# Optimization experiments

Hardware: AMD Instinct MI355X
Metric: run time of the kernel (lower is better)

The kernel has to match this reference:

```python
import jax, jax.numpy as jnp
import numpy as np

B, T, W = 64, 64, 20
VIDEO_DIM = 1024
JOINT_DIM = 1024
K, STRIDE = 4, 4
MARGIN = 0.2
EPS = 1e-8


def _l2norm(x, axis=-1):
    n = jnp.sqrt(jnp.sum(x * x, axis=axis, keepdims=True))
    return x / jnp.maximum(n, EPS)


def _conv1d(x, w, b, stride):
    # x: (B, C, L), w: (O, I, K) -> (B, O, L_out), VALID padding (padding=0)
    y = jax.lax.conv_general_dilated(x, w, (stride,), 'VALID',
                                     dimension_numbers=('NCH', 'OIH', 'NCH'))
    return y + b[None, :, None]


def _diag_loss(scores, margin):
    # faithful port of diag(): row/column margin costs with zeroed diagonal
    b = scores.shape[0]
    d = jnp.diagonal(scores)
    off = 1.0 - jnp.eye(b, dtype=scores.dtype)
    cost_s = jnp.maximum(margin + scores - d[:, None], 0.0) * off
    cost_im = jnp.maximum(margin + scores - d[None, :], 0.0) * off
    return cost_s.sum() / b + cost_im.sum() / b


def setup_inputs() -> dict:
    key = jax.random.key(0)
    ks = jax.random.split(key, 10)
    def g(k, shape, scale=0.02):
        return jax.random.normal(k, shape, dtype=jnp.float32) * scale
    return dict(
        video=jax.random.normal(ks[0], (B, T, VIDEO_DIM), dtype=jnp.float32),
        words=jax.random.normal(ks[1], (B, W, JOINT_DIM), dtype=jnp.float32),
        w_masks=jnp.ones((B, W), dtype=jnp.int32),
        sentences=jax.random.normal(ks[2], (B, JOINT_DIM), dtype=jnp.float32),
        conv0_w=g(ks[3], (JOINT_DIM, VIDEO_DIM, K)),
        conv0_b=jnp.zeros((JOINT_DIM,), jnp.float32),
        conv1_w=g(ks[4], (JOINT_DIM, JOINT_DIM, K)),
        conv1_b=jnp.zeros((JOINT_DIM,), jnp.float32),
        conv2_w=g(ks[5], (JOINT_DIM, JOINT_DIM, K)),
        conv2_b=jnp.zeros((JOINT_DIM,), jnp.float32),
        conv1d_w=g(ks[6], (JOINT_DIM, JOINT_DIM, 1)),
        conv1d_b=jnp.zeros((JOINT_DIM,), jnp.float32),
        fc_w=g(ks[7], (JOINT_DIM, JOINT_DIM)),
        fc_b=jnp.zeros((JOINT_DIM,), jnp.float32),
    )


def reference(video, words, w_masks, sentences,
              conv0_w, conv0_b, conv1_w, conv1_b, conv2_w, conv2_b,
              conv1d_w, conv1d_b, fc_w, fc_b):
    # Vectorizes the original per-sample python loop over the pair axes (i=sentence, j=video).
    x = jnp.transpose(video, (0, 2, 1))          # (B, C, T)
    wmask = (w_masks > 0)                        # (B, W)
    conv_params = [(conv0_w, conv0_b), (conv1_w, conv1_b), (conv2_w, conv2_b)]
    sims = []
    v_tmp = x
    for cw, cb in conv_params:
        v_tmp = jax.nn.relu(_conv1d(v_tmp, cw, cb, STRIDE))
        v = jnp.transpose(_conv1d(v_tmp, conv1d_w, conv1d_b, 1), (0, 2, 1))  # (B, Tl, D)
        # frame_by_word: masked softmax attention of frames over words
        att = jnp.einsum('jtd,iwd->ijtw', v, words)            # (i, j, Tl, W)
        att = jnp.where(wmask[:, None, None, :], att, -1e30)
        att = jax.nn.softmax(att, axis=-1)
        v_s = jnp.einsum('ijtw,iwd->ijtd', att, words)         # attended word ctx
        # cosine sim of l2-normed vectors == dot product
        sim = jnp.einsum('jtd,ijtd->ijt', _l2norm(v), _l2norm(v_s))
        sims.append(sim)
    score_all = jnp.concatenate(sims, axis=2)    # (B, B, T_total=21)
    # torch code sorts descending then means over dim 1 -> mean is sort-invariant
    scores = score_all.mean(axis=2)              # (B, B) local scores
    positive_map = score_all[jnp.arange(B), jnp.arange(B)]     # (B, T_total)
    # global branch: final conv output has length 1 -> squeeze
    g_v = _l2norm(v_tmp[:, :, 0] @ fc_w.T + fc_b)              # (B, D), unit norm
    g_scores = _l2norm(sentences) @ g_v.T                      # [i, j] = cos(g_v[j], sent[i])
    loss = _diag_loss(scores, MARGIN) + _diag_loss(g_scores, MARGIN)
    return loss, positive_map
```

## Files before the change

kernel.cpp:

```cpp
#include <hip/hip_runtime.h>
#include <cmath>
#include <cstdint>


typedef __bf16 bf16_t;
typedef bf16_t bf16x8 __attribute__((ext_vector_type(8)));
typedef bf16_t bf16x4 __attribute__((ext_vector_type(4)));
typedef bf16_t bf16x2 __attribute__((ext_vector_type(2)));
typedef float  f32x4  __attribute__((ext_vector_type(4)));

#define CP0_SL   1048576

#define MFMA16(a,b,c) __builtin_amdgcn_mfma_f32_16x16x32_bf16(a, b, c, 0, 0, 0)

__device__ __forceinline__ void gload_lds16(const void* g, void* l) {
    __builtin_amdgcn_global_load_lds(
        (const __attribute__((address_space(1))) void*)g,
        (__attribute__((address_space(3))) void*)l, 16, 0, 0);
}

__device__ __forceinline__ int swz(int r, int c) { return (r * 8 + (c ^ (r & 7))) * 8; }

__device__ __forceinline__ void wtrans4(const float* __restrict__ w,
                                        bf16_t* __restrict__ wt,
                                        int o0, int tid, bf16_t* lds )
{
    #pragma unroll
    for (int oo = 0; oo < 4; oo++) {
        const float* src = w + ((size_t)(o0 + oo) << 12);
        #pragma unroll
        for (int q = 0; q < 2; q++) {
            f32x4 va = *(const f32x4*)(src + tid * 16 + q * 8);
            f32x4 vb = *(const f32x4*)(src + tid * 16 + q * 8 + 4);
            int ib = tid * 4 + 2 * q;
            #pragma unroll
            for (int k = 0; k < 4; k++) {
                bf16x2 p2 = { (bf16_t)va[k], (bf16_t)vb[k] };
                *(bf16x2*)(lds + oo * 4096 + k * 1024 + ib) = p2;
            }
        }
    }
    __syncthreads();
    #pragma unroll
    for (int oo = 0; oo < 4; oo++) {
        bf16x8 v0 = *(bf16x8*)(lds + oo * 4096 + tid * 16);
        bf16x8 v1 = *(bf16x8*)(lds + oo * 4096 + tid * 16 + 8);
        bf16_t* dst = wt + ((size_t)(o0 + oo) << 12) + tid * 16;
        *(bf16x8*)dst       = v0;
        *(bf16x8*)(dst + 8) = v1;
    }
}

__device__ __forceinline__ void cast8(const float* __restrict__ s,
                                      bf16_t* __restrict__ d, int idx8)
{
    f32x4 a = *(const f32x4*)(s + (size_t)idx8 * 8);
    f32x4 b = *(const f32x4*)(s + (size_t)idx8 * 8 + 4);
    bf16x8 o;
    #pragma unroll
    for (int e = 0; e < 4; e++) { o[e] = (bf16_t)a[e]; o[4 + e] = (bf16_t)b[e]; }
    *(bf16x8*)(d + (size_t)idx8 * 8) = o;
}

__device__ __forceinline__ void gemm64(
    const bf16_t* __restrict__ A, const bf16_t* __restrict__ B,
    int Nc, int K, int m0A, int n0B, int k0, int nIt, int m0C, int n0C,
    bf16_t* sA, bf16_t* sB,
    float* __restrict__ Cf, const float* __restrict__ bias, bf16_t* __restrict__ Dbf,
    int relu)
{
    const int tid  = threadIdx.x;
    const int lane = tid & 63, wave = tid >> 6;
    const int sr = tid >> 3, pc = tid & 7, lc = pc ^ (sr & 7);
    const bf16_t* Ag = A + (size_t)(m0A + sr) * K + k0 + lc * 8;
    const bf16_t* Bg = B + (size_t)(n0B + sr) * K + k0 + lc * 8;
    const size_t rowskip = (size_t)32 * K;
    const int wr = (wave >> 1) * 32, wc = (wave & 1) * 32;
    const int fm = lane & 15, cb = lane >> 4;
    int offA[2][2], offB[2][2];
    #pragma unroll
    for (int h = 0; h < 2; h++) {
        offA[h][0] = swz(wr +      fm, cb + h * 4);
        offA[h][1] = swz(wr + 16 + fm, cb + h * 4);
        offB[h][0] = swz(wc +      fm, cb + h * 4);
        offB[h][1] = swz(wc + 16 + fm, cb + h * 4);
    }
    f32x4 acc[2][2];
    #pragma unroll
    for (int a = 0; a < 2; a++)
        #pragma unroll
        for (int b = 0; b < 2; b++) acc[a][b] = (f32x4){0.f, 0.f, 0.f, 0.f};

    gload_lds16(Ag,           sA + tid * 8);
    gload_lds16(Ag + rowskip, sA + 2048 + tid * 8);
    gload_lds16(Bg,           sB + tid * 8);
    gload_lds16(Bg + rowskip, sB + 2048 + tid * 8);
    for (int it = 0; it < nIt; ++it) {
        const int buf = it & 1;
        const bf16_t* cA = sA + buf * 4096;
        const bf16_t* cB = sB + buf * 4096;
        __syncthreads();
        if (it + 1 < nIt) {
            const bf16_t* a = Ag + (it + 1) * 64;
            const bf16_t* b = Bg + (it + 1) * 64;
            bf16_t* dA = sA + (buf ^ 1) * 4096;
            bf16_t* dB = sB + (buf ^ 1) * 4096;
            gload_lds16(a,           dA + tid * 8);
            gload_lds16(a + rowskip, dA + 2048 + tid * 8);
            gload_lds16(b,           dB + tid * 8);
            gload_lds16(b + rowskip, dB + 2048 + tid * 8);
        }
        #pragma unroll
        for (int h = 0; h < 2; h++) {
            bf16x8 a0 = *(const bf16x8*)&cA[offA[h][0]];
            bf16x8 a1 = *(const bf16x8*)&cA[offA[h][1]];
            bf16x8 b0 = *(const bf16x8*)&cB[offB[h][0]];
            bf16x8 b1 = *(const bf16x8*)&cB[offB[h][1]];
            acc[0][0] = MFMA16(a0, b0, acc[0][0]);
            acc[0][1] = MFMA16(a0, b1, acc[0][1]);
            acc[1][0] = MFMA16(a1, b0, acc[1][0]);
            acc[1][1] = MFMA16(a1, b1, acc[1][1]);
        }
    }
    #pragma unroll
    for (int im = 0; im < 2; im++)
        #pragma unroll
        for (int rr = 0; rr < 4; rr++) {
            int gm = m0C + wr + im * 16 + cb * 4 + rr;
            #pragma unroll
            for (int in_ = 0; in_ < 2; in_++) {
                int cg = n0C + wc + in_ * 16 + fm;
                float v = acc[im][in_][rr];
                if (bias) v += bias[cg];
                if (relu) v = fmaxf(v, 0.f);
                if (Dbf) Dbf[(size_t)gm * Nc + cg] = (bf16_t)v;
                else     Cf[(size_t)gm * Nc + cg] = v;
            }
        }
}

__device__ __forceinline__ void rownorm_row(const bf16_t* __restrict__ VCb,
                                            float* __restrict__ VN, int r, int tid)
{
    const int lane = tid & 63;
    const bf16_t* x = VCb + ((size_t)r << 10) + lane * 16;
    bf16x8 v0 = *(const bf16x8*)x, v1 = *(const bf16x8*)(x + 8);
    float s = 0.f;
    #pragma unroll
    for (int e = 0; e < 8; e++) {
        float a = (float)v0[e], b = (float)v1[e];
        s += a * a + b * b;
    }
    #pragma unroll
    for (int o = 32; o; o >>= 1) s += __shfl_xor(s, o, 64);
    if (lane == 0) VN[r] = sqrtf(s);
}

__device__ __forceinline__ void sim_compute(
    int i, int c, const float* __restrict__ CPat, const float* __restrict__ VN,
    const float* Gs, const float* msk, float* __restrict__ SA)
{
    float s[20], p[20];
    float mx = -1e30f;
    #pragma unroll
    for (int w = 0; w < 20; w++) {
        s[w] = CPat[(size_t)(i * 20 + w) * 1344 + c];
        if (msk[w] != 0.f) mx = fmaxf(mx, s[w]);
    }
    float denom = 0.f, num = 0.f;
    #pragma unroll
    for (int w = 0; w < 20; w++) {
        p[w] = (msk[w] != 0.f) ? __expf(s[w] - mx) : 0.f;
        denom += p[w];
        num   += p[w] * s[w];
    }
    float quad = 0.f;
    #pragma unroll
    for (int w = 0; w < 20; w++) {
        float cc = 0.f;
        #pragma unroll
        for (int w2 = 0; w2 < 20; w2++) cc += Gs[w * 20 + w2] * p[w2];
        quad += p[w] * cc;
    }
    float dot = num / denom;
    float vsn = sqrtf(fmaxf(quad, 0.f)) / denom;
    float sim = dot / (fmaxf(VN[c], 1e-8f) * fmaxf(vsn, 1e-8f));
    int j, t;
    if (c < 1024)      { j = c >> 4;          t = c & 15; }
    else if (c < 1280) { j = (c - 1024) >> 2; t = 16 + ((c - 1024) & 3); }
    else               { j = c - 1280;        t = 20; }
    SA[((size_t)i * 64 + j) * 21 + t] = sim;
}

__global__ __launch_bounds__(256) void prep0_kernel(
    const float* __restrict__ c0w, bf16_t* __restrict__ WT0,
    const float* __restrict__ video, bf16_t* __restrict__ Vb)
{
    __shared__ __align__(16) bf16_t lds[16384];
    int bx = blockIdx.x;
    if (bx < 256) wtrans4(c0w, WT0, bx * 4, threadIdx.x, lds);
    else          cast8(video, Vb, (bx - 256) * 256 + threadIdx.x);
}

__global__ __launch_bounds__(256) void d2_kernel(
    const bf16_t* __restrict__ Vb, const bf16_t* __restrict__ WT0, float* __restrict__ CP0,
    const float* __restrict__ c1w, const float* __restrict__ c2w,
    bf16_t* __restrict__ WT1, bf16_t* __restrict__ WT2,
    const float* __restrict__ words, bf16_t* __restrict__ Wordsb,
    const float* __restrict__ c1dw, bf16_t* __restrict__ C1b,
    const float* __restrict__ fcw, bf16_t* __restrict__ Fb)
{
    __shared__ __align__(16) bf16_t smem[32768];
    const int bx = blockIdx.x, tid = threadIdx.x;
    if (bx < 256) {
        bf16_t* sA = smem;
        bf16_t* sB = smem + 16384;
        const int z = bx >> 6, rem = bx & 63, xt = rem & 7, yt = rem >> 3;
        const int m0 = xt * 128, n0 = yt * 128, k0 = z * 1024;
        const int lane = tid & 63, wave = tid >> 6;
        const int sr = tid >> 3, pc = tid & 7, lc = pc ^ (sr & 7);
        const bf16_t* Ag = Vb  + (size_t)(m0 + sr) * 4096 + k0 + lc * 8;
        const bf16_t* Bg = WT0 + (size_t)(n0 + sr) * 4096 + k0 + lc * 8;
        const size_t rowskip = (size_t)32 * 4096;
        const int wrow = (wave >> 1) * 64, wcol = (wave & 1) * 64;
        const int fm = lane & 15, cb = lane >> 4;
        int offA[2][4], offB[2][4];
        #pragma unroll
        for (int h = 0; h < 2; h++)
            #pragma unroll
            for (int m = 0; m < 4; m++) {
                offA[h][m] = swz(wrow + m * 16 + fm, cb + h * 4);
                offB[h][m] = swz(wcol + m * 16 + fm, cb + h * 4);
            }
        f32x4 acc[4][4];
        #pragma unroll
        for (int m = 0; m < 4; m++)
            #pragma unroll
            for (int n = 0; n < 4; n++) acc[m][n] = (f32x4){0.f, 0.f, 0.f, 0.f};

        #pragma unroll
        for (int g = 0; g < 4; g++) {
            gload_lds16(Ag + g * rowskip, &sA[tid * 8 + g * 2048]);
            gload_lds16(Bg + g * rowskip, &sB[tid * 8 + g * 2048]);
        }
        for (int it = 0; it < 16; ++it) {
            const int buf = it & 1;
            __syncthreads();
            if (it < 15) {
                const bf16_t* a = Ag + (it + 1) * 64;
                const bf16_t* b = Bg + (it + 1) * 64;
                #pragma unroll
                for (int g = 0; g < 4; g++) {
                    gload_lds16(a + g * rowskip, &sA[(buf ^ 1) * 8192 + tid * 8 + g * 2048]);
                    gload_lds16(b + g * rowskip, &sB[(buf ^ 1) * 8192 + tid * 8 + g * 2048]);
                }
            }
            #pragma unroll
            for (int h = 0; h < 2; h++) {
                bf16x8 av[4], bv[4];
                #pragma unroll
                for (int m = 0; m < 4; m++) {
                    av[m] = *(const bf16x8*)&sA[buf * 8192 + offA[h][m]];
                    bv[m] = *(const bf16x8*)&sB[buf * 8192 + offB[h][m]];
                }
                #pragma unroll
                for (int m = 0; m < 4; m++)
                    #pragma unroll
                    for (int n = 0; n < 4; n++)
                        acc[m][n] = MFMA16(av[m], bv[n], acc[m][n]);
            }
        }
        float* Cz = CP0 + (size_t)z * CP0_SL;
        #pragma unroll
        for (int m = 0; m < 4; m++)
            #pragma unroll
            for (int rr = 0; rr < 4; rr++) {
                int gm = m0 + wrow + m * 16 + cb * 4 + rr;
                #pragma unroll
                for (int n = 0; n < 4; n++) {
                    int cg = n0 + wcol + n * 16 + fm;
                    Cz[(size_t)gm * 1024 + cg] = acc[m][n][rr];
                }
            }
    } else if (bx < 768) {
        int b2 = bx - 256;
        if (b2 < 256) wtrans4(c1w, WT1, b2 * 4, tid, smem);
        else          wtrans4(c2w, WT2, (b2 - 256) * 4, tid, smem);
    } else {
        int b2 = bx - 768;
        if (b2 < 640)       cast8(words, Wordsb, b2 * 256 + tid);
        else if (b2 < 1152) cast8(c1dw, C1b, (b2 - 640) * 256 + tid);
        else                cast8(fcw, Fb, (b2 - 1152) * 256 + tid);
    }
}

__global__ __launch_bounds__(256) void d3_kernel(
    const float* __restrict__ CP0, const float* __restrict__ c0b,
    bf16_t* __restrict__ Astack, const bf16_t* __restrict__ Wordsb,
    float* __restrict__ GR)
{
    int bx = blockIdx.x, tid = threadIdx.x;
    if (bx < 512) {
        int idx8 = bx * 256 + tid;
        size_t base = (size_t)idx8 * 8;
        int nb = (int)(base & 1023);
        f32x4 s0 = *(const f32x4*)(c0b + nb);
        f32x4 s1 = *(const f32x4*)(c0b + nb + 4);
        #pragma unroll
        for (int z = 0; z < 4; z++) {
            const float* p = CP0 + (size_t)z * CP0_SL + base;
            s0 += *(const f32x4*)p;
            s1 += *(const f32x4*)(p + 4);
        }
        bf16x8 o;
        #pragma unroll
        for (int e = 0; e < 4; e++) {
            o[e]     = (bf16_t)fmaxf(s0[e], 0.f);
            o[4 + e] = (bf16_t)fmaxf(s1[e], 0.f);
        }
        *(bf16x8*)(Astack + base) = o;
    } else {
        int g = bx - 512;
        int i = g / 100, piece = g % 100;
        int wave = tid >> 6, lane = tid & 63;
        int pair = piece * 4 + wave;
        int w = pair / 20, w2 = pair % 20;
        const bf16_t* a = Wordsb + (((size_t)i * 20 + w)  << 10) + lane * 16;
        const bf16_t* b = Wordsb + (((size_t)i * 20 + w2) << 10) + lane * 16;
        bf16x8 a0 = *(const bf16x8*)a, a1 = *(const bf16x8*)(a + 8);
        bf16x8 b0 = *(const bf16x8*)b, b1 = *(const bf16x8*)(b + 8);
        float s = 0.f;
        #pragma unroll
        for (int e = 0; e < 8; e++)
            s += (float)a0[e] * (float)b0[e] + (float)a1[e] * (float)b1[e];
        #pragma unroll
        for (int o = 32; o; o >>= 1) s += __shfl_xor(s, o, 64);
        if (lane == 0) GR[(size_t)i * 400 + pair] = s;
    }
}

__global__ __launch_bounds__(256) void d4_kernel(
    const bf16_t* __restrict__ Astack, const bf16_t* __restrict__ WT1,
    const float* __restrict__ c1b, bf16_t* __restrict__ A2b,
    const bf16_t* __restrict__ C1b, const float* __restrict__ c1db,
    bf16_t* __restrict__ VCb)
{
    __shared__ __align__(16) bf16_t smem[16384];
    bf16_t* sA = smem; bf16_t* sB = smem + 8192;
    int bx = blockIdx.x;
    if (bx < 64) {
        int xt = bx & 3, yt = bx >> 2;
        gemm64(Astack, WT1, 1024, 4096, xt * 64, yt * 64, 0, 64,
               xt * 64, yt * 64, sA, sB, nullptr, c1b, A2b, 1);
    } else {
        int b2 = bx - 64;
        int xt = b2 & 15, yt = b2 >> 4;
        gemm64(Astack, C1b, 1024, 1024, xt * 64, yt * 64, 0, 16,
               xt * 64, yt * 64, sA, sB, nullptr, c1db, VCb, 0);
    }
}

__global__ __launch_bounds__(256) void d6_kernel(
    const bf16_t* __restrict__ A2b, const bf16_t* __restrict__ WT2,
    const float* __restrict__ c2b, bf16_t* __restrict__ A3b,
    const bf16_t* __restrict__ C1b, const float* __restrict__ c1db,
    const bf16_t* __restrict__ Wordsb, bf16_t* __restrict__ VCb,
    float* __restrict__ CPat, float* __restrict__ VN)
{
    __shared__ __align__(16) bf16_t smem[16384];
    bf16_t* sA = smem; bf16_t* sB = smem + 8192;
    int bx = blockIdx.x, tid = threadIdx.x;
    if (bx < 16) {
        gemm64(A2b, WT2, 1024, 4096, 0, bx * 64, 0, 64,
               0, bx * 64, sA, sB, nullptr, c2b, A3b, 1);
    } else if (bx < 336) {
        int g = bx - 16;
        int xt = g % 20, yt = g / 20;
        gemm64(Wordsb, VCb, 1344, 1024, xt * 64, yt * 64, 0, 16,
               xt * 64, yt * 64, sA, sB, CPat, nullptr, nullptr, 0);
    } else if (bx < 400) {
        int g = bx - 336;
        int xt = g & 3, yt = g >> 2;
        gemm64(A2b, C1b, 1024, 1024, xt * 64, yt * 64, 0, 16,
               1024 + xt * 64, yt * 64, sA, sB, nullptr, c1db, VCb, 0);
    } else {
        int r = (bx - 400) * 4 + (tid >> 6);
        rownorm_row(VCb, VN, r, tid);
    }
}

__global__ __launch_bounds__(256) void d7_kernel(
    const bf16_t* __restrict__ A3b, const bf16_t* __restrict__ C1b,
    const bf16_t* __restrict__ Fb,
    const float* __restrict__ c1db, const float* __restrict__ fcb,
    bf16_t* __restrict__ VCb, float* __restrict__ GV,
    const bf16_t* __restrict__ Wordsb, float* __restrict__ CPat,
    const float* __restrict__ GR, float* __restrict__ VN,
    const int* __restrict__ wmask, float* __restrict__ SA)
{
    __shared__ __align__(16) bf16_t smem[16384];
    bf16_t* sA = smem; bf16_t* sB = smem + 8192;
    const int bx = blockIdx.x, tid = threadIdx.x;
    if (bx < 16) {
        gemm64(A3b, C1b, 1024, 1024, 0, bx * 64, 0, 16,
               1280, bx * 64, sA, sB, nullptr, c1db, VCb, 0);
    } else if (bx < 32) {
        int yt = bx - 16;
        gemm64(A3b, Fb, 1024, 1024, 0, yt * 64, 0, 16,
               0, yt * 64, sA, sB, GV, fcb, nullptr, 0);
    } else if (bx < 112) {
        int g = bx - 32;
        int xt = g % 20, yt = g / 20;
        gemm64(Wordsb, VCb, 1344, 1024, xt * 64, 1024 + yt * 64, 0, 16,
               xt * 64, 1024 + yt * 64, sA, sB, CPat, nullptr, nullptr, 0);
    } else if (bx < 368) {
        int s = bx - 112;
        int i = s >> 2, seg = s & 3;
        float* Gs  = (float*)smem;
        float* msk = Gs + 400;
        for (int q = tid; q < 400; q += 256) Gs[q] = GR[(size_t)i * 400 + q];
        if (tid < 20) msk[tid] = (wmask[i * 20 + tid] != 0) ? 1.f : 0.f;
        __syncthreads();
        sim_compute(i, seg * 256 + tid, CPat, VN, Gs, msk, SA);
    } else {
        int r = 1024 + (bx - 368) * 4 + (tid >> 6);
        rownorm_row(VCb, VN, r, tid);
    }
}

__global__ __launch_bounds__(256) void d8_kernel(
    const bf16_t* __restrict__ Wordsb, const bf16_t* __restrict__ VCb,
    float* __restrict__ CPat, float* __restrict__ VN,
    const float* __restrict__ sent, const float* __restrict__ GV,
    float* __restrict__ GS, const float* __restrict__ GR,
    const int* __restrict__ wmask, float* __restrict__ SA)
{
    __shared__ __align__(16) bf16_t smem[16384];
    bf16_t* sA = smem; bf16_t* sB = smem + 8192;
    int bx = blockIdx.x, tid = threadIdx.x;
    if (bx < 20) {
        gemm64(Wordsb, VCb, 1344, 1024, bx * 64, 1280, 0, 16,
               bx * 64, 1280, sA, sB, CPat, nullptr, nullptr, 0);
    } else if (bx < 36) {
        int r = 1280 + (bx - 20) * 4 + (tid >> 6);
        rownorm_row(VCb, VN, r, tid);
    } else if (bx < 1060) {
        int item = (bx - 36) * 4 + (tid >> 6);
        int i = item >> 6, j = item & 63;
        int lane = tid & 63;
        const float* a = sent + (size_t)i * 1024;
        const float* b = GV + (size_t)j * 1024;
        float sab = 0.f, saa = 0.f, sbb = 0.f;
        #pragma unroll
        for (int q = 0; q < 16; q++) {
            int d = lane + 64 * q;
            float av = a[d], bv = b[d];
            sab += av * bv; saa += av * av; sbb += bv * bv;
        }
        #pragma unroll
        for (int o = 32; o; o >>= 1) {
            sab += __shfl_xor(sab, o, 64);
            saa += __shfl_xor(saa, o, 64);
            sbb += __shfl_xor(sbb, o, 64);
        }
        if (lane == 0)
            GS[item] = sab / (fmaxf(sqrtf(saa), 1e-8f) * fmaxf(sqrtf(sbb), 1e-8f));
    } else {
        int i = bx - 1060;
        float* Gs  = (float*)smem;
        float* msk = Gs + 400;
        for (int q = tid; q < 400; q += 256) Gs[q] = GR[(size_t)i * 400 + q];
        if (tid < 20) msk[tid] = (wmask[i * 20 + tid] != 0) ? 1.f : 0.f;
        __syncthreads();
        sim_compute(i, 1024 + tid, CPat, VN, Gs, msk, SA);
    }
}

__global__ __launch_bounds__(256) void d9_kernel(
    const float* __restrict__ CPat, const float* __restrict__ GR,
    const float* __restrict__ VN, const int* __restrict__ wmask,
    float* __restrict__ SA)
{
    __shared__ float Gs[400];
    __shared__ float msk[20];
    int i = blockIdx.x, tid = threadIdx.x;
    for (int q = tid; q < 400; q += 256) Gs[q] = GR[(size_t)i * 400 + q];
    if (tid < 20) msk[tid] = (wmask[i * 20 + tid] != 0) ? 1.f : 0.f;
    __syncthreads();
    if (tid < 64) sim_compute(i, 1280 + tid, CPat, VN, Gs, msk, SA);
}

__global__ __launch_bounds__(256) void d10_kernel(
    const float* __restrict__ SA, float* __restrict__ SC, float* __restrict__ out)
{
    int idx = blockIdx.x * 256 + threadIdx.x;
    int i = idx >> 6, j = idx & 63;
    const float* row = SA + (size_t)idx * 21;
    float s = 0.f;
    #pragma unroll
    for (int t = 0; t < 21; t++) s += row[t];
    SC[idx] = s * (1.0f / 21.0f);
    if (i == j) {
        #pragma unroll
        for (int t = 0; t < 21; t++) out[1 + i * 21 + t] = row[t];
    }
}

__global__ __launch_bounds__(256) void loss_kernel(
    const float* __restrict__ SC_, const float* __restrict__ GS_,
    float* __restrict__ out)
{
    __shared__ float d1[64], d2[64], red[4];
    int tid = threadIdx.x;
    if (tid < 64) { d1[tid] = SC_[tid * 65]; d2[tid] = GS_[tid * 65]; }
    __syncthreads();
    float acc = 0.f;
    for (int idx = tid; idx < 4096; idx += 256) {
        int i = idx >> 6, j = idx & 63;
        if (i != j) {
            float s = SC_[idx];
            acc += fmaxf(0.2f + s - d1[i], 0.f) + fmaxf(0.2f + s - d1[j], 0.f);
            float g = GS_[idx];
            acc += fmaxf(0.2f + g - d2[i], 0.f) + fmaxf(0.2f + g - d2[j], 0.f);
        }
    }
    #pragma unroll
    for (int o = 32; o; o >>= 1) acc += __shfl_xor(acc, o, 64);
    if ((tid & 63) == 0) red[tid >> 6] = acc;
    __syncthreads();
    if (tid == 0) out[0] = (red[0] + red[1] + red[2] + red[3]) * (1.0f / 64.0f);
}

extern "C" void kernel_launch(void* const* d_in, const int* in_sizes, int n_in,
                              void* d_out, int out_size, void* d_ws, size_t ws_size,
                              hipStream_t stream)
{
    const float* video     = (const float*)d_in[0];
    const float* words     = (const float*)d_in[1];
    const int*   w_masks   = (const int*)  d_in[2];
    const float* sentences = (const float*)d_in[3];
    const float* conv0_w   = (const float*)d_in[4];
    const float* conv0_b   = (const float*)d_in[5];
    const float* conv1_w   = (const float*)d_in[6];
    const float* conv1_b   = (const float*)d_in[7];
    const float* conv2_w   = (const float*)d_in[8];
    const float* conv2_b   = (const float*)d_in[9];
    const float* conv1d_w  = (const float*)d_in[10];
    const float* conv1d_b  = (const float*)d_in[11];
    const float* fc_w      = (const float*)d_in[12];
    const float* fc_b      = (const float*)d_in[13];
    float* out = (float*)d_out;
    float* ws = (float*)d_ws;

    bf16_t* WT0    = (bf16_t*)(ws + 0);
    bf16_t* WT1    = (bf16_t*)(ws + 2097152);
    bf16_t* WT2    = (bf16_t*)(ws + 4194304);
    bf16_t* Vb     = (bf16_t*)(ws + 6291456);
    bf16_t* Wordsb = (bf16_t*)(ws + 8388608);
    bf16_t* C1b    = (bf16_t*)(ws + 9043968);
    bf16_t* Fb     = (bf16_t*)(ws + 9568256);
    bf16_t* Astack = (bf16_t*)(ws + 10092544);
    bf16_t* A2b    = (bf16_t*)(ws + 10616832);
    bf16_t* A3b    = (bf16_t*)(ws + 10747904);
    bf16_t* VCb    = (bf16_t*)(ws + 10780672);
    float*  CP0    = ws + 11468800;
    float*  CPat   = ws + 15663104;
    float*  VN     = ws + 17383424;
    float*  GR     = ws + 17384768;
    float*  SA     = ws + 17410368;
    float*  SC     = ws + 17496384;
    float*  GV     = ws + 17500480;
    float*  GS     = ws + 17566016;

    dim3 blk(256);

    prep0_kernel<<<2304, blk, 0, stream>>>(conv0_w, WT0, video, Vb);
    d2_kernel<<<2432, blk, 0, stream>>>(Vb, WT0, CP0, conv1_w, conv2_w, WT1, WT2,
                                        words, Wordsb, conv1d_w, C1b, fc_w, Fb);
    d3_kernel<<<6912, blk, 0, stream>>>(CP0, conv0_b, Astack, Wordsb, GR);
    d4_kernel<<<320, blk, 0, stream>>>(Astack, WT1, conv1_b, A2b, C1b, conv1d_b, VCb);
    d6_kernel<<<656, blk, 0, stream>>>(A2b, WT2, conv2_b, A3b, C1b, conv1d_b,
                                       Wordsb, VCb, CPat, VN);
    d7_kernel<<<432, blk, 0, stream>>>(A3b, C1b, Fb, conv1d_b, fc_b,
                                       VCb, GV, Wordsb, CPat, GR, VN, w_masks, SA);
    d8_kernel<<<1124, blk, 0, stream>>>(Wordsb, VCb, CPat, VN, sentences, GV, GS,
                                        GR, w_masks, SA);
    d9_kernel<<<64, blk, 0, stream>>>(CPat, GR, VN, w_masks, SA);
    d10_kernel<<<16, blk, 0, stream>>>(SA, SC, out);
    loss_kernel<<<1, blk, 0, stream>>>(SC, GS, out);
}
```

Measured before the change: 274.9 us.

## Double GEMM K-step to 128 and fold score reduction into sim via atomics

The shared GEMM routine now stages 128-wide K slices per iteration with a 16-chunk swizzle. This halves the number of loop iterations and barriers in every GEMM call, at the cost of twice the LDS per block. Separately, the per-pair score buffer and its reduction kernel are removed. Each sim value is instead atomically added, pre-scaled, into the score matrix, with the diagonal written directly to the output, and the score matrix is zeroed by extra blocks in an earlier kernel. The higher LDS use may reduce occupancy, and the atomics make the summation order nondeterministic.

After: 247.5 us. -10.0%, faster.

```diff
diff --git a/kernel.cpp b/kernel.cpp
--- a/kernel.cpp
+++ b/kernel.cpp
@@ -19,7 +19,8 @@
         (__attribute__((address_space(3))) void*)l, 16, 0, 0);
 }
 
-__device__ __forceinline__ int swz(int r, int c) { return (r * 8 + (c ^ (r & 7))) * 8; }
+__device__ __forceinline__ int swz(int r, int c)    { return (r * 8  + (c ^ (r & 7)))  * 8; }
+__device__ __forceinline__ int swz128(int r, int c) { return (r * 16 + (c ^ (r & 15))) * 8; }
 
 __device__ __forceinline__ void wtrans4(const float* __restrict__ w,
                                         bf16_t* __restrict__ wt,
@@ -71,19 +72,22 @@
 {
     const int tid  = threadIdx.x;
     const int lane = tid & 63, wave = tid >> 6;
-    const int sr = tid >> 3, pc = tid & 7, lc = pc ^ (sr & 7);
-    const bf16_t* Ag = A + (size_t)(m0A + sr) * K + k0 + lc * 8;
-    const bf16_t* Bg = B + (size_t)(n0B + sr) * K + k0 + lc * 8;
-    const size_t rowskip = (size_t)32 * K;
+    const bf16_t* AgP[4]; const bf16_t* BgP[4];
+    #pragma unroll
+    for (int g = 0; g < 4; g++) {
+        int q = g * 256 + tid, row = q >> 4, pcc = q & 15, lcc = pcc ^ (row & 15);
+        AgP[g] = A + (size_t)(m0A + row) * K + k0 + lcc * 8;
+        BgP[g] = B + (size_t)(n0B + row) * K + k0 + lcc * 8;
+    }
     const int wr = (wave >> 1) * 32, wc = (wave & 1) * 32;
     const int fm = lane & 15, cb = lane >> 4;
-    int offA[2][2], offB[2][2];
-    #pragma unroll
-    for (int h = 0; h < 2; h++) {
-        offA[h][0] = swz(wr +      fm, cb + h * 4);
-        offA[h][1] = swz(wr + 16 + fm, cb + h * 4);
-        offB[h][0] = swz(wc +      fm, cb + h * 4);
-        offB[h][1] = swz(wc + 16 + fm, cb + h * 4);
+    int offA[4][2], offB[4][2];
+    #pragma unroll
+    for (int h = 0; h < 4; h++) {
+        offA[h][0] = swz128(wr +      fm, cb + h * 4);
+        offA[h][1] = swz128(wr + 16 + fm, cb + h * 4);
+        offB[h][0] = swz128(wc +      fm, cb + h * 4);
+        offB[h][1] = swz128(wc + 16 + fm, cb + h * 4);
     }
     f32x4 acc[2][2];
     #pragma unroll
@@ -91,27 +95,27 @@
         #pragma unroll
         for (int b = 0; b < 2; b++) acc[a][b] = (f32x4){0.f, 0.f, 0.f, 0.f};
 
-    gload_lds16(Ag,           sA + tid * 8);
-    gload_lds16(Ag + rowskip, sA + 2048 + tid * 8);
-    gload_lds16(Bg,           sB + tid * 8);
-    gload_lds16(Bg + rowskip, sB + 2048 + tid * 8);
+    #pragma unroll
+    for (int g = 0; g < 4; g++) {
+        gload_lds16(AgP[g], sA + (g * 256 + tid) * 8);
+        gload_lds16(BgP[g], sB + (g * 256 + tid) * 8);
+    }
     for (int it = 0; it < nIt; ++it) {
         const int buf = it & 1;
-        const bf16_t* cA = sA + buf * 4096;
-        const bf16_t* cB = sB + buf * 4096;
+        const bf16_t* cA = sA + buf * 8192;
+        const bf16_t* cB = sB + buf * 8192;
         __syncthreads();
         if (it + 1 < nIt) {
-            const bf16_t* a = Ag + (it + 1) * 64;
-            const bf16_t* b = Bg + (it + 1) * 64;
-            bf16_t* dA = sA + (buf ^ 1) * 4096;
-            bf16_t* dB = sB + (buf ^ 1) * 4096;
-            gload_lds16(a,           dA + tid * 8);
-            gload_lds16(a + rowskip, dA + 2048 + tid * 8);
-            gload_lds16(b,           dB + tid * 8);
-            gload_lds16(b + rowskip, dB + 2048 + tid * 8);
-        }
-        #pragma unroll
-        for (int h = 0; h < 2; h++) {
+            bf16_t* dA = sA + (buf ^ 1) * 8192;
+            bf16_t* dB = sB + (buf ^ 1) * 8192;
+            #pragma unroll
+            for (int g = 0; g < 4; g++) {
+                gload_lds16(AgP[g] + (it + 1) * 128, dA + (g * 256 + tid) * 8);
+                gload_lds16(BgP[g] + (it + 1) * 128, dB + (g * 256 + tid) * 8);
+            }
+        }
+        #pragma unroll
+        for (int h = 0; h < 4; h++) {
             bf16x8 a0 = *(const bf16x8*)&cA[offA[h][0]];
             bf16x8 a1 = *(const bf16x8*)&cA[offA[h][1]];
             bf16x8 b0 = *(const bf16x8*)&cB[offB[h][0]];
@@ -158,7 +162,8 @@
 
 __device__ __forceinline__ void sim_compute(
     int i, int c, const float* __restrict__ CPat, const float* __restrict__ VN,
-    const float* Gs, const float* msk, float* __restrict__ SA)
+    const float* Gs, const float* msk,
+    float* __restrict__ SC, float* __restrict__ out)
 {
     float s[20], p[20];
     float mx = -1e30f;
@@ -189,7 +194,8 @@
     if (c < 1024)      { j = c >> 4;          t = c & 15; }
     else if (c < 1280) { j = (c - 1024) >> 2; t = 16 + ((c - 1024) & 3); }
     else               { j = c - 1280;        t = 20; }
-    SA[((size_t)i * 64 + j) * 21 + t] = sim;
+    atomicAdd(SC + i * 64 + j, sim * (1.0f / 21.0f));
+    if (i == j) out[1 + i * 21 + t] = sim;
 }
 
 __global__ __launch_bounds__(256) void prep0_kernel(
@@ -297,7 +303,7 @@
 __global__ __launch_bounds__(256) void d3_kernel(
     const float* __restrict__ CP0, const float* __restrict__ c0b,
     bf16_t* __restrict__ Astack, const bf16_t* __restrict__ Wordsb,
-    float* __restrict__ GR)
+    float* __restrict__ GR, float* __restrict__ SC)
 {
     int bx = blockIdx.x, tid = threadIdx.x;
     if (bx < 512) {
@@ -319,7 +325,7 @@
             o[4 + e] = (bf16_t)fmaxf(s1[e], 0.f);
         }
         *(bf16x8*)(Astack + base) = o;
-    } else {
+    } else if (bx < 6912) {
         int g = bx - 512;
         int i = g / 100, piece = g % 100;
         int wave = tid >> 6, lane = tid & 63;
@@ -336,6 +342,9 @@
         #pragma unroll
         for (int o = 32; o; o >>= 1) s += __shfl_xor(s, o, 64);
         if (lane == 0) GR[(size_t)i * 400 + pair] = s;
+    } else {
+        int idx = (bx - 6912) * 1024 + tid * 4;
+        *(f32x4*)(SC + idx) = (f32x4){0.f, 0.f, 0.f, 0.f};
     }
 }
 
@@ -345,17 +354,17 @@
     const bf16_t* __restrict__ C1b, const float* __restrict__ c1db,
     bf16_t* __restrict__ VCb)
 {
-    __shared__ __align__(16) bf16_t smem[16384];
-    bf16_t* sA = smem; bf16_t* sB = smem + 8192;
+    __shared__ __align__(16) bf16_t smem[32768];
+    bf16_t* sA = smem; bf16_t* sB = smem + 16384;
     int bx = blockIdx.x;
     if (bx < 64) {
         int xt = bx & 3, yt = bx >> 2;
-        gemm64(Astack, WT1, 1024, 4096, xt * 64, yt * 64, 0, 64,
+        gemm64(Astack, WT1, 1024, 4096, xt * 64, yt * 64, 0, 32,
                xt * 64, yt * 64, sA, sB, nullptr, c1b, A2b, 1);
     } else {
         int b2 = bx - 64;
         int xt = b2 & 15, yt = b2 >> 4;
-        gemm64(Astack, C1b, 1024, 1024, xt * 64, yt * 64, 0, 16,
+        gemm64(Astack, C1b, 1024, 1024, xt * 64, yt * 64, 0, 8,
                xt * 64, yt * 64, sA, sB, nullptr, c1db, VCb, 0);
     }
 }
@@ -367,21 +376,21 @@
     const bf16_t* __restrict__ Wordsb, bf16_t* __restrict__ VCb,
     float* __restrict__ CPat, float* __restrict__ VN)
 {
-    __shared__ __align__(16) bf16_t smem[16384];
-    bf16_t* sA = smem; bf16_t* sB = smem + 8192;
+    __shared__ __align__(16) bf16_t smem[32768];
+    bf16_t* sA = smem; bf16_t* sB = smem + 16384;
     int bx = blockIdx.x, tid = threadIdx.x;
     if (bx < 16) {
-        gemm64(A2b, WT2, 1024, 4096, 0, bx * 64, 0, 64,
+        gemm64(A2b, WT2, 1024, 4096, 0, bx * 64, 0, 32,
                0, bx * 64, sA, sB, nullptr, c2b, A3b, 1);
     } else if (bx < 336) {
         int g = bx - 16;
         int xt = g % 20, yt = g / 20;
-        gemm64(Wordsb, VCb, 1344, 1024, xt * 64, yt * 64, 0, 16,
+        gemm64(Wordsb, VCb, 1344, 1024, xt * 64, yt * 64, 0, 8,
                xt * 64, yt * 64, sA, sB, CPat, nullptr, nullptr, 0);
     } else if (bx < 400) {
         int g = bx - 336;
         int xt = g & 3, yt = g >> 2;
-        gemm64(A2b, C1b, 1024, 1024, xt * 64, yt * 64, 0, 16,
+        gemm64(A2b, C1b, 1024, 1024, xt * 64, yt * 64, 0, 8,
                1024 + xt * 64, yt * 64, sA, sB, nullptr, c1db, VCb, 0);
     } else {
         int r = (bx - 400) * 4 + (tid >> 6);
@@ -396,22 +405,22 @@
     bf16_t* __restrict__ VCb, float* __restrict__ GV,
     const bf16_t* __restrict__ Wordsb, float* __restrict__ CPat,
     const float* __restrict__ GR, float* __restrict__ VN,
-    const int* __restrict__ wmask, float* __restrict__ SA)
-{
-    __shared__ __align__(16) bf16_t smem[16384];
-    bf16_t* sA = smem; bf16_t* sB = smem + 8192;
+    const int* __restrict__ wmask, float* __restrict__ SC, float* __restrict__ out)
+{
+    __shared__ __align__(16) bf16_t smem[32768];
+    bf16_t* sA = smem; bf16_t* sB = smem + 16384;
     const int bx = blockIdx.x, tid = threadIdx.x;
     if (bx < 16) {
-        gemm64(A3b, C1b, 1024, 1024, 0, bx * 64, 0, 16,
+        gemm64(A3b, C1b, 1024, 1024, 0, bx * 64, 0, 8,
                1280, bx * 64, sA, sB, nullptr, c1db, VCb, 0);
     } else if (bx < 32) {
         int yt = bx - 16;
-        gemm64(A3b, Fb, 1024, 1024, 0, yt * 64, 0, 16,
+        gemm64(A3b, Fb, 1024, 1024, 0, yt * 64, 0, 8,
                0, yt * 64, sA, sB, GV, fcb, nullptr, 0);
     } else if (bx < 112) {
         int g = bx - 32;
         int xt = g % 20, yt = g / 20;
-        gemm64(Wordsb, VCb, 1344, 1024, xt * 64, 1024 + yt * 64, 0, 16,
+        gemm64(Wordsb, VCb, 1344, 1024, xt * 64, 1024 + yt * 64, 0, 8,
                xt * 64, 1024 + yt * 64, sA, sB, CPat, nullptr, nullptr, 0);
     } else if (bx < 368) {
         int s = bx - 112;
@@ -421,7 +430,7 @@
         for (int q = tid; q < 400; q += 256) Gs[q] = GR[(size_t)i * 400 + q];
         if (tid < 20) msk[tid] = (wmask[i * 20 + tid] != 0) ? 1.f : 0.f;
         __syncthreads();
-        sim_compute(i, seg * 256 + tid, CPat, VN, Gs, msk, SA);
+        sim_compute(i, seg * 256 + tid, CPat, VN, Gs, msk, SC, out);
     } else {
         int r = 1024 + (bx - 368) * 4 + (tid >> 6);
         rownorm_row(VCb, VN, r, tid);
@@ -433,13 +442,13 @@
     float* __restrict__ CPat, float* __restrict__ VN,
     const float* __restrict__ sent, const float* __restrict__ GV,
     float* __restrict__ GS, const float* __restrict__ GR,
-    const int* __restrict__ wmask, float* __restrict__ SA)
-{
-    __shared__ __align__(16) bf16_t smem[16384];
-    bf16_t* sA = smem; bf16_t* sB = smem + 8192;
+    const int* __restrict__ wmask, float* __restrict__ SC, float* __restrict__ out)
+{
+    __shared__ __align__(16) bf16_t smem[32768];
+    bf16_t* sA = smem; bf16_t* sB = smem + 16384;
     int bx = blockIdx.x, tid = threadIdx.x;
     if (bx < 20) {
-        gemm64(Wordsb, VCb, 1344, 1024, bx * 64, 1280, 0, 16,
+        gemm64(Wordsb, VCb, 1344, 1024, bx * 64, 1280, 0, 8,
                bx * 64, 1280, sA, sB, CPat, nullptr, nullptr, 0);
     } else if (bx < 36) {
         int r = 1280 + (bx - 20) * 4 + (tid >> 6);
@@ -472,14 +481,14 @@
         for (int q = tid; q < 400; q += 256) Gs[q] = GR[(size_t)i * 400 + q];
         if (tid < 20) msk[tid] = (wmask[i * 20 + tid] != 0) ? 1.f : 0.f;
         __syncthreads();
-        sim_compute(i, 1024 + tid, CPat, VN, Gs, msk, SA);
+        sim_compute(i, 1024 + tid, CPat, VN, Gs, msk, SC, out);
     }
 }
 
 __global__ __launch_bounds__(256) void d9_kernel(
     const float* __restrict__ CPat, const float* __restrict__ GR,
     const float* __restrict__ VN, const int* __restrict__ wmask,
-    float* __restrict__ SA)
+    float* __restrict__ SC, float* __restrict__ out)
 {
     __shared__ float Gs[400];
     __shared__ float msk[20];
@@ -487,23 +496,7 @@
     for (int q = tid; q < 400; q += 256) Gs[q] = GR[(size_t)i * 400 + q];
     if (tid < 20) msk[tid] = (wmask[i * 20 + tid] != 0) ? 1.f : 0.f;
     __syncthreads();
-    if (tid < 64) sim_compute(i, 1280 + tid, CPat, VN, Gs, msk, SA);
-}
-
-__global__ __launch_bounds__(256) void d10_kernel(
-    const float* __restrict__ SA, float* __restrict__ SC, float* __restrict__ out)
-{
-    int idx = blockIdx.x * 256 + threadIdx.x;
-    int i = idx >> 6, j = idx & 63;
-    const float* row = SA + (size_t)idx * 21;
-    float s = 0.f;
-    #pragma unroll
-    for (int t = 0; t < 21; t++) s += row[t];
-    SC[idx] = s * (1.0f / 21.0f);
-    if (i == j) {
-        #pragma unroll
-        for (int t = 0; t < 21; t++) out[1 + i * 21 + t] = row[t];
-    }
+    if (tid < 64) sim_compute(i, 1280 + tid, CPat, VN, Gs, msk, SC, out);
 }
 
 __global__ __launch_bounds__(256) void loss_kernel(
@@ -567,25 +560,23 @@
     float*  CPat   = ws + 15663104;
     float*  VN     = ws + 17383424;
     float*  GR     = ws + 17384768;
-    float*  SA     = ws + 17410368;
-    float*  SC     = ws + 17496384;
-    float*  GV     = ws + 17500480;
-    float*  GS     = ws + 17566016;
+    float*  SC     = ws + 17410368;
+    float*  GV     = ws + 17414464;
+    float*  GS     = ws + 17480000;
 
     dim3 blk(256);
 
     prep0_kernel<<<2304, blk, 0, stream>>>(conv0_w, WT0, video, Vb);
     d2_kernel<<<2432, blk, 0, stream>>>(Vb, WT0, CP0, conv1_w, conv2_w, WT1, WT2,
                                         words, Wordsb, conv1d_w, C1b, fc_w, Fb);
-    d3_kernel<<<6912, blk, 0, stream>>>(CP0, conv0_b, Astack, Wordsb, GR);
+    d3_kernel<<<6916, blk, 0, stream>>>(CP0, conv0_b, Astack, Wordsb, GR, SC);
     d4_kernel<<<320, blk, 0, stream>>>(Astack, WT1, conv1_b, A2b, C1b, conv1d_b, VCb);
     d6_kernel<<<656, blk, 0, stream>>>(A2b, WT2, conv2_b, A3b, C1b, conv1d_b,
                                        Wordsb, VCb, CPat, VN);
     d7_kernel<<<432, blk, 0, stream>>>(A3b, C1b, Fb, conv1d_b, fc_b,
-                                       VCb, GV, Wordsb, CPat, GR, VN, w_masks, SA);
+                                       VCb, GV, Wordsb, CPat, GR, VN, w_masks, SC, out);
     d8_kernel<<<1124, blk, 0, stream>>>(Wordsb, VCb, CPat, VN, sentences, GV, GS,
-                                        GR, w_masks, SA);
-    d9_kernel<<<64, blk, 0, stream>>>(CPat, GR, VN, w_masks, SA);
-    d10_kernel<<<16, blk, 0, stream>>>(SA, SC, out);
+                                        GR, w_masks, SC, out);
+    d9_kernel<<<64, blk, 0, stream>>>(CPat, GR, VN, w_masks, SC, out);
     loss_kernel<<<1, blk, 0, stream>>>(SC, GS, out);
 }
```
